# Kernel optimization log

Measured on AMD Instinct MI355X. Metric: run time of the kernel, lower is better.

The kernel has to match this reference:

```python
import math
import jax, jax.numpy as jnp
import numpy as np

B, S, DIM, H = 16, 1024, 1024, 16
HD = DIM // H            # head_dim = 64
ROPE_DIM = HD // 2       # 32; per-axis rotary dim
FT = 32                  # ft_seq_len, FT*FT == S
PT = 16                  # pt_seq_len
THETA = 10000.0
EPS = 1e-6


def _rope_cos_sin():
    # freqs_for='lang'
    freqs = 1.0 / THETA ** (jnp.arange(0, ROPE_DIM, 2, dtype=jnp.float32) / ROPE_DIM)  # [ROPE_DIM//2]
    t = jnp.arange(FT, dtype=jnp.float32) / FT * PT                                    # [FT]
    fs = jnp.einsum('n,f->nf', t, freqs)                                               # [FT, ROPE_DIM//2]
    fs = jnp.repeat(fs, 2, axis=-1)                                                    # [FT, ROPE_DIM]
    fh = jnp.broadcast_to(fs[:, None, :], (FT, FT, ROPE_DIM))
    fw = jnp.broadcast_to(fs[None, :, :], (FT, FT, ROPE_DIM))
    f = jnp.concatenate([fh, fw], axis=-1).reshape(-1, 2 * ROPE_DIM)                   # [S, HD]
    return jnp.cos(f), jnp.sin(f)


def _rotate_half(x):
    x1, x2 = jnp.split(x, 2, axis=-1)
    return jnp.concatenate((-x2, x1), axis=-1)


def _rms_norm(x, w):
    xf = x.astype(jnp.float32)
    var = jnp.mean(jnp.square(xf), axis=-1, keepdims=True)
    return (w * (xf * jax.lax.rsqrt(var + EPS))).astype(x.dtype)


def setup_inputs() -> dict:
    key = jax.random.key(0)
    ks = jax.random.split(key, 4)
    sd = 1.0 / math.sqrt(DIM)
    return {
        'x': jax.random.normal(ks[0], (B, S, DIM), dtype=jnp.float32),
        'w_qkv': jax.random.normal(ks[1], (DIM, 3 * DIM), dtype=jnp.float32) * sd,
        'b_qkv': jnp.zeros((3 * DIM,), dtype=jnp.float32),
        'q_norm_w': jnp.ones((HD,), dtype=jnp.float32),
        'k_norm_w': jnp.ones((HD,), dtype=jnp.float32),
        'w_out': jax.random.normal(ks[2], (DIM, DIM), dtype=jnp.float32) * sd,
        'b_out': jnp.zeros((DIM,), dtype=jnp.float32),
    }


def reference(x, w_qkv, b_qkv, q_norm_w, k_norm_w, w_out, b_out):
    cos, sin = _rope_cos_sin()                    # [S, HD] each
    cos = cos[None, None].astype(x.dtype)
    sin = sin[None, None].astype(x.dtype)

    qkv = x @ w_qkv + b_qkv                       # [B,S,3*DIM]
    qkv = qkv.reshape(B, S, 3, H, HD).transpose(2, 0, 3, 1, 4)  # [3,B,H,S,HD]
    q, k, v = qkv[0], qkv[1], qkv[2]

    q = _rms_norm(q, q_norm_w)
    k = _rms_norm(k, k_norm_w)

    q = q * cos + _rotate_half(q) * sin
    k = k * cos + _rotate_half(k) * sin

    scale = 1.0 / math.sqrt(HD)
    logits = jnp.einsum('bhqd,bhkd->bhqk', q.astype(jnp.float32), k.astype(jnp.float32)) * scale
    attn = jax.nn.softmax(logits, axis=-1).astype(x.dtype)
    out = jnp.einsum('bhqk,bhkd->bhqd', attn, v)  # [B,H,S,HD]

    out = out.transpose(0, 2, 1, 3).reshape(B, S, DIM)
    return out @ w_out + b_out
```

## Files before the change

kernel.cpp:

```cpp
#include <hip/hip_runtime.h>
#include <cstdint>
#include <cstddef>

#define B_    16
#define S_    1024
#define DIM_  1024
#define H_    16
#define HD_   64
#define TDIM  3072

typedef unsigned short ushort_t;
typedef unsigned int   uint_t;
typedef __attribute__((ext_vector_type(8)))  short s8v;
typedef __attribute__((ext_vector_type(4)))  float f32x4;
typedef __attribute__((ext_vector_type(16))) float f32x16;

__device__ __forceinline__ float b2f(ushort_t u) {
    union { uint_t i; float f; } t; t.i = (uint_t)u << 16; return t.f;
}
__device__ __forceinline__ ushort_t f2b(float f) {
    union { float f; uint_t i; } t; t.f = f;
    uint_t r = t.i + 0x7FFFu + ((t.i >> 16) & 1u);
    return (ushort_t)(r >> 16);
}
__device__ __forceinline__ uint_t cvt_pk_bf16(float a, float b) {
    uint_t r;
    asm("v_cvt_pk_bf16_f32 %0, %1, %2" : "=v"(r) : "v"(a), "v"(b));
    return r;
}

__device__ __forceinline__ f32x4 mfma_bf16(s8v a, s8v b, f32x4 c) {
    asm volatile("v_mfma_f32_16x16x32_bf16 %0, %1, %2, %0" : "+v"(c) : "v"(a), "v"(b));
    return c;
}
__device__ __forceinline__ f32x16 mfma32_bf16(s8v a, s8v b, f32x16 c) {
    asm volatile("v_mfma_f32_32x32x16_bf16 %0, %1, %2, %0" : "+v"(c) : "v"(a), "v"(b));
    return c;
}

__device__ __forceinline__ void gload16(const void* g, void* l) {
    __builtin_amdgcn_global_load_lds(
        (const __attribute__((address_space(1))) uint_t*)g,
        (__attribute__((address_space(3))) uint_t*)l, 16, 0, 0);
}

__device__ __forceinline__ void bar() {
    asm volatile("" ::: "memory");
    __builtin_amdgcn_s_barrier();
    asm volatile("" ::: "memory");
}
__device__ __forceinline__ void wait_vm0() {
    asm volatile("s_waitcnt vmcnt(0)" ::: "memory");
}
__device__ __forceinline__ void wait_vm4() {
    asm volatile("s_waitcnt vmcnt(4)" ::: "memory");
}

__global__ __launch_bounds__(256) void f32_to_bf16_vec(const float* __restrict__ src,
                                                       short* __restrict__ dst, int n8) {
    int i = blockIdx.x * 256 + threadIdx.x;
    if (i < n8) {
        float4 a = *(const float4*)(src + (size_t)i * 8);
        float4 b = *(const float4*)(src + (size_t)i * 8 + 4);
        s8v t;
        t[0] = (short)f2b(a.x); t[1] = (short)f2b(a.y);
        t[2] = (short)f2b(a.z); t[3] = (short)f2b(a.w);
        t[4] = (short)f2b(b.x); t[5] = (short)f2b(b.y);
        t[6] = (short)f2b(b.z); t[7] = (short)f2b(b.w);
        *(s8v*)(dst + (size_t)i * 8) = t;
    }
}

__global__ __launch_bounds__(256) void rope_tables(float* __restrict__ cos_t,
                                                   float* __restrict__ sin_t) {
    int idx = blockIdx.x * 256 + threadIdx.x;
    int s = idx >> 6;
    int d = idx & 63;
    int pos = (d < 32) ? (s >> 5) : (s & 31);
    int i   = (d & 31) >> 1;
    float freq  = expf(-(float)i * 0.5756462732485115f);
    float angle = (float)pos * 0.5f * freq;
    cos_t[idx] = cosf(angle);
    sin_t[idx] = sinf(angle);
}

__global__ __launch_bounds__(256) void transpose_to_bf16(const float* __restrict__ Wsrc,
                                                         short* __restrict__ WT,
                                                         int K, int N) {
    __shared__ float t[32][33];
    int tx = threadIdx.x & 31, ty = threadIdx.x >> 5;
    int n0 = blockIdx.x * 32, k0 = blockIdx.y * 32;
#pragma unroll
    for (int i = 0; i < 4; ++i)
        t[ty + 8 * i][tx] = Wsrc[(size_t)(k0 + ty + 8 * i) * N + n0 + tx];
    __syncthreads();
#pragma unroll
    for (int i = 0; i < 4; ++i)
        WT[(size_t)(n0 + ty + 8 * i) * K + k0 + tx] = (short)f2b(t[tx][ty + 8 * i]);
}

template<typename CT, bool NORM>
__global__ __launch_bounds__(512) void gemm8ph(
        const short* __restrict__ A, const short* __restrict__ BT,
        const float* __restrict__ bias, CT* __restrict__ C,
        int M, int N, int K, int NX,
        const float* __restrict__ qw, const float* __restrict__ kw,
        const float* __restrict__ cos_t, const float* __restrict__ sin_t) {
    __shared__ short As[2][256 * 64];
    __shared__ short Bs[3][256 * 64];

    const int tid  = threadIdx.x;
    const int w    = tid >> 6;
    const int lane = tid & 63;
    const int l15  = lane & 15, lg = lane >> 4;
    const int wm = w >> 2, wn = w & 3;

    const int nwg  = gridDim.x;
    const int cpx  = nwg >> 3;
    const int wgid = (blockIdx.x & 7) * cpx + (blockIdx.x >> 3);
    const int bx = wgid % NX, by = wgid / NX;
    const int m0 = by * 256, n0 = bx * 256;

    const int NT = K >> 6;

    const int sgrow = w * 8 + (lane >> 3);
    const int ksrc  = (((lane & 7) ^ (lane >> 3)) * 8);

    auto stageA = [&](int t, int buf) {
        const size_t k0 = (size_t)t * 64;
#pragma unroll
        for (int j = 0; j < 4; ++j)
            gload16(A + (size_t)(m0 + j * 64 + sgrow) * K + k0 + ksrc,
                    &As[buf][(j * 64 + w * 8) * 64]);
    };
    auto stageB = [&](int t, int buf) {
        const size_t k0 = (size_t)t * 64;
#pragma unroll
        for (int j = 0; j < 4; ++j)
            gload16(BT + (size_t)(n0 + j * 64 + sgrow) * K + k0 + ksrc,
                    &Bs[buf][(j * 64 + w * 8) * 64]);
    };

    const int swz = l15 & 7;

    auto rdA = [&](int buf, int mh, s8v (&dst)[4][2]) {
#pragma unroll
        for (int i = 0; i < 4; ++i) {
            int row = wm * 128 + mh * 64 + i * 16 + l15;
#pragma unroll
            for (int kk = 0; kk < 2; ++kk)
                dst[i][kk] = *(const s8v*)&As[buf][row * 64 + (((kk * 4 + lg) ^ swz) * 8)];
        }
    };
    auto rdB = [&](int buf, int nh, s8v (&dst)[4][2]) {
#pragma unroll
        for (int ni = 0; ni < 2; ++ni) {
            int row = wn * 64 + (nh * 2 + ni) * 16 + l15;
#pragma unroll
            for (int kk = 0; kk < 2; ++kk)
                dst[nh * 2 + ni][kk] = *(const s8v*)&Bs[buf][row * 64 + (((kk * 4 + lg) ^ swz) * 8)];
        }
    };

    stageA(0, 0);
    stageB(0, 0);
    stageB(1, 1);
    wait_vm4();
    bar();

    s8v a0[4][2], a1[4][2], bb[4][2];
    rdA(0, 0, a0);
    rdB(0, 0, bb);
    rdB(0, 1, bb);
    rdA(0, 1, a1);

    f32x4 acc[8][4] = {};

    int bufB = 0;
    for (int t = 0; t < NT; ++t) {
        const int bufA  = t & 1;
        const int nbufB = (bufB == 2) ? 0 : bufB + 1;
        const int sbufB = (nbufB == 2) ? 0 : nbufB + 1;

        if (t + 1 < NT) stageA(t + 1, bufA ^ 1);
        if (t + 2 < NT) stageB(t + 2, sbufB);

        __builtin_amdgcn_s_setprio(1);
#pragma unroll
        for (int i = 0; i < 4; ++i)
#pragma unroll
            for (int ni = 0; ni < 2; ++ni)
#pragma unroll
                for (int kk = 0; kk < 2; ++kk)
                    acc[i][ni] = mfma_bf16(a0[i][kk], bb[ni][kk], acc[i][ni]);
        __builtin_amdgcn_s_setprio(0);

        __builtin_amdgcn_s_setprio(1);
#pragma unroll
        for (int i = 0; i < 4; ++i)
#pragma unroll
            for (int ni = 2; ni < 4; ++ni)
#pragma unroll
                for (int kk = 0; kk < 2; ++kk)
                    acc[i][ni] = mfma_bf16(a0[i][kk], bb[ni][kk], acc[i][ni]);
        __builtin_amdgcn_s_setprio(0);

        __builtin_amdgcn_s_setprio(1);
#pragma unroll
        for (int i = 0; i < 4; ++i)
#pragma unroll
            for (int ni = 0; ni < 2; ++ni)
#pragma unroll
                for (int kk = 0; kk < 2; ++kk)
                    acc[4 + i][ni] = mfma_bf16(a1[i][kk], bb[ni][kk], acc[4 + i][ni]);
        __builtin_amdgcn_s_setprio(0);

        if (t < NT - 2) wait_vm4(); else wait_vm0();
        bar();

        if (t + 1 < NT) {
            rdA(bufA ^ 1, 0, a0);
            rdB(nbufB, 0, bb);
        }

        __builtin_amdgcn_s_setprio(1);
#pragma unroll
        for (int i = 0; i < 4; ++i)
#pragma unroll
            for (int ni = 2; ni < 4; ++ni)
#pragma unroll
                for (int kk = 0; kk < 2; ++kk)
                    acc[4 + i][ni] = mfma_bf16(a1[i][kk], bb[ni][kk], acc[4 + i][ni]);
        __builtin_amdgcn_s_setprio(0);

        if (t + 1 < NT) {
            rdB(nbufB, 1, bb);
            rdA(bufA ^ 1, 1, a1);
        }
        bufB = nbufB;
    }

    const int colbase = n0 + wn * 64;
    if constexpr (NORM) {
        if (colbase < 2048) {
            const float* nw = (colbase < 1024) ? qw : kw;
            float wv[4], bv[4];
#pragma unroll
            for (int ni = 0; ni < 4; ++ni) {
                wv[ni] = nw[16 * ni + l15];
                bv[ni] = bias[colbase + 16 * ni + l15];
            }
#pragma unroll
            for (int mi = 0; mi < 8; ++mi) {
#pragma unroll
                for (int r = 0; r < 4; ++r) {
                    int row = m0 + wm * 128 + mi * 16 + lg * 4 + r;
                    int s = row & (S_ - 1);
                    float v[4];
#pragma unroll
                    for (int ni = 0; ni < 4; ++ni) v[ni] = acc[mi][ni][r] + bv[ni];
                    float ss = v[0]*v[0] + v[1]*v[1] + v[2]*v[2] + v[3]*v[3];
                    ss += __shfl_xor(ss, 1);
                    ss += __shfl_xor(ss, 2);
                    ss += __shfl_xor(ss, 4);
                    ss += __shfl_xor(ss, 8);
                    float rms = rsqrtf(ss * (1.0f / 64.0f) + 1e-6f);
                    float xn[4];
#pragma unroll
                    for (int ni = 0; ni < 4; ++ni) xn[ni] = v[ni] * rms * wv[ni];
#pragma unroll
                    for (int ni = 0; ni < 4; ++ni) {
                        int d = 16 * ni + l15;
                        float c  = cos_t[s * 64 + d];
                        float sn = sin_t[s * 64 + d];
                        float rot = (ni < 2) ? -xn[ni + 2] : xn[ni - 2];
                        C[(size_t)row * N + colbase + d] = (short)f2b(xn[ni] * c + rot * sn);
                    }
                }
            }
            return;
        }
    }
#pragma unroll
    for (int ni = 0; ni < 4; ++ni) {
        float bvv = bias[colbase + 16 * ni + l15];
#pragma unroll
        for (int mi = 0; mi < 8; ++mi) {
#pragma unroll
            for (int r = 0; r < 4; ++r) {
                size_t row = (size_t)(m0 + wm * 128 + mi * 16 + lg * 4 + r);
                int    col = colbase + 16 * ni + l15;
                float v = acc[mi][ni][r] + bvv;
                if constexpr (sizeof(CT) == 4) C[row * N + col] = v;
                else                           C[row * N + col] = (short)f2b(v);
            }
        }
    }
}

__global__ __launch_bounds__(256) void attn_mfma(const short* __restrict__ qkv,
                                                 short* __restrict__ attn) {
    __shared__ ushort_t pool[8192];

    const float SC = 0.18033688011112042f;
    const float M_ = 12.0f;

    const int tid  = threadIdx.x;
    const int w    = tid >> 6;
    const int lane = tid & 63;
    const int l31  = lane & 31, l5 = lane >> 5;

    const int bid = blockIdx.x;
    const int xcd = bid & 7;
    const int jj_ = bid >> 3;
    const int bh  = xcd * 32 + (jj_ >> 3);
    const int b   = bh >> 4, h = bh & 15;
    const int q0  = (jj_ & 7) * 128;

    const short* qbase = qkv + (size_t)b * S_ * TDIM + h * HD_;
    const short* kb_ = qbase + DIM_;
    const short* vb_ = qbase + 2 * DIM_;

    ushort_t* Ks = pool;
    ushort_t* Vt = pool + 4096;

    s8v qf[4];
#pragma unroll
    for (int kc = 0; kc < 4; ++kc)
        qf[kc] = *(const s8v*)(qbase + (size_t)(q0 + w * 32 + l31) * TDIM + kc * 16 + l5 * 8);

    f32x16 of0 = {}, of1 = {};
    float l_s = 0.f;

    const int kr   = tid >> 3;
    const int kch  = (((tid & 7) ^ (kr & 7)) << 3);
    const int va   = tid & 7;
    const int vkp  = tid >> 3;
    const int vp8  = va * 8;
    const int k2    = 2 * vkp;
    const int kperm = (k2 & 0x33) | ((k2 & 4) << 1) | ((k2 & 8) >> 1);
    const int rsw   = l31 & 7;
    const int vrx   = (l31 & 7) ^ (l31 >> 3);

    s8v kA, kB, vA, vB;
    auto prefetch = [&](int kt) {
        const short* kbt = kb_ + (size_t)kt * 64 * TDIM;
        const short* vbt = vb_ + (size_t)kt * 64 * TDIM;
        kA = *(const s8v*)(kbt + (size_t)kr * TDIM + (tid & 7) * 8);
        kB = *(const s8v*)(kbt + (size_t)(kr + 32) * TDIM + (tid & 7) * 8);
        vA = *(const s8v*)(vbt + (size_t)k2 * TDIM + vp8);
        vB = *(const s8v*)(vbt + (size_t)(k2 + 1) * TDIM + vp8);
    };
    prefetch(0);

    for (int kt = 0; kt < 16; ++kt) {
        *(s8v*)&Ks[kr * 64 + kch]        = kA;
        *(s8v*)&Ks[(kr + 32) * 64 + kch] = kB;
#pragma unroll
        for (int j = 0; j < 8; ++j) {
            uint_t pk = (ushort_t)vA[j] | ((uint_t)(ushort_t)vB[j] << 16);
            int pcol = ((((kperm >> 3) ^ j ^ va) << 3) | (kperm & 7));
            *(uint_t*)&Vt[(vp8 + j) * 64 + pcol] = pk;
        }
        __syncthreads();

        if (kt < 15) prefetch(kt + 1);

        f32x16 st0 = {}, st1 = {};
        __builtin_amdgcn_s_setprio(1);
#pragma unroll
        for (int kc = 0; kc < 4; ++kc) {
            int pc = (((2 * kc + l5) ^ rsw) << 3);
            s8v kf0 = *(const s8v*)&Ks[l31 * 64 + pc];
            s8v kf1 = *(const s8v*)&Ks[(32 + l31) * 64 + pc];
            st0 = mfma32_bf16(kf0, qf[kc], st0);
            st1 = mfma32_bf16(kf1, qf[kc], st1);
        }
        __builtin_amdgcn_s_setprio(0);

        float la = 0.f, lb = 0.f, lc = 0.f, ld = 0.f;
#pragma unroll
        for (int r = 0; r < 16; r += 2) {
            float p00 = exp2f(__builtin_fmaf(st0[r],     SC, -M_));
            float p01 = exp2f(__builtin_fmaf(st0[r + 1], SC, -M_));
            float p10 = exp2f(__builtin_fmaf(st1[r],     SC, -M_));
            float p11 = exp2f(__builtin_fmaf(st1[r + 1], SC, -M_));
            st0[r] = p00; st0[r + 1] = p01;
            st1[r] = p10; st1[r + 1] = p11;
            la += p00; lb += p01; lc += p10; ld += p11;
        }
        float ls = (la + lb) + (lc + ld);
        ls += __shfl_xor(ls, 32);
        l_s += ls;

        uint_t P20[8], P21[8];
#pragma unroll
        for (int i = 0; i < 8; ++i) {
            P20[i] = cvt_pk_bf16(st0[2 * i], st0[2 * i + 1]);
            P21[i] = cvt_pk_bf16(st1[2 * i], st1[2 * i + 1]);
        }

        __builtin_amdgcn_s_setprio(1);
#pragma unroll
        for (int kb = 0; kb < 2; ++kb) {
            const uint_t* P2 = kb ? P21 : P20;
#pragma unroll
            for (int c = 0; c < 2; ++c) {
                union { uint_t u[4]; s8v v; } pf;
                pf.u[0] = P2[4 * c + 0];
                pf.u[1] = P2[4 * c + 1];
                pf.u[2] = P2[4 * c + 2];
                pf.u[3] = P2[4 * c + 3];

                int pc0 = (((4 * kb + 2 * c + l5) ^ vrx) << 3);
                int pc1 = pc0 ^ 32;
                s8v vf0 = *(const s8v*)&Vt[l31 * 64 + pc0];
                s8v vf1 = *(const s8v*)&Vt[(32 + l31) * 64 + pc1];
                of0 = mfma32_bf16(vf0, pf.v, of0);
                of1 = mfma32_bf16(vf1, pf.v, of1);
            }
        }
        __builtin_amdgcn_s_setprio(0);
        __syncthreads();
    }

    float inv = 1.0f / l_s;
    ushort_t* OL = pool + w * 2048;
#pragma unroll
    for (int r = 0; r < 16; r += 2) {
        int d = (r & 3) + 8 * (r >> 2) + 4 * l5;
        uint_t p0 = cvt_pk_bf16(of0[r] * inv, of0[r + 1] * inv);
        uint_t p1 = cvt_pk_bf16(of1[r] * inv, of1[r + 1] * inv);
        int c0 = d, c1 = 32 + d;
        int pc0 = (((c0 >> 3) ^ (l31 & 7)) << 3) | (c0 & 7);
        int pc1 = (((c1 >> 3) ^ (l31 & 7)) << 3) | (c1 & 7);
        *(uint_t*)&OL[l31 * 64 + pc0] = p0;
        *(uint_t*)&OL[l31 * 64 + pc1] = p1;
    }
#pragma unroll
    for (int i = 0; i < 4; ++i) {
        int idx = lane + i * 64;
        int row = idx >> 3, ch = idx & 7;
        int pch = ((ch ^ (row & 7)) << 3);
        *(s8v*)&attn[((size_t)b * S_ + q0 + w * 32 + row) * DIM_ + h * HD_ + ch * 8] =
            *(const s8v*)&OL[row * 64 + pch];
    }
}

extern "C" void kernel_launch(void* const* d_in, const int* in_sizes, int n_in,
                              void* d_out, int out_size, void* d_ws, size_t ws_size,
                              hipStream_t stream) {
    const float* x        = (const float*)d_in[0];
    const float* w_qkv    = (const float*)d_in[1];
    const float* b_qkv    = (const float*)d_in[2];
    const float* q_norm_w = (const float*)d_in[3];
    const float* k_norm_w = (const float*)d_in[4];
    const float* w_out    = (const float*)d_in[5];
    const float* b_out    = (const float*)d_in[6];
    float* out = (float*)d_out;

    const size_t OFF_QKV = 0;
    const size_t OFF_ATT = 100663296;
    const size_t OFF_XB  = OFF_ATT + 33554432;
    const size_t OFF_WQ  = OFF_XB + 33554432;
    const size_t OFF_WO  = OFF_WQ + 6291456;
    const size_t OFF_CT  = OFF_WO + 2097152;
    const size_t OFF_ST  = OFF_CT + 262144;
    const size_t NEED    = OFF_ST + 262144;

    if (ws_size < NEED) {
        hipMemsetAsync(d_out, 0, (size_t)out_size * sizeof(float), stream);
        return;
    }

    char* ws = (char*)d_ws;
    short* qkv   = (short*)(ws + OFF_QKV);
    short* attnb = (short*)(ws + OFF_ATT);
    short* xb    = (short*)(ws + OFF_XB);
    short* wqkvT = (short*)(ws + OFF_WQ);
    short* woutT = (short*)(ws + OFF_WO);
    float* cos_t = (float*)(ws + OFF_CT);
    float* sin_t = (float*)(ws + OFF_ST);

    rope_tables<<<dim3(256), dim3(256), 0, stream>>>(cos_t, sin_t);
    f32_to_bf16_vec<<<dim3(8192), dim3(256), 0, stream>>>(x, xb, 2097152);
    transpose_to_bf16<<<dim3(96, 32), dim3(256), 0, stream>>>(w_qkv, wqkvT, 1024, 3072);
    transpose_to_bf16<<<dim3(32, 32), dim3(256), 0, stream>>>(w_out, woutT, 1024, 1024);

    gemm8ph<short, true><<<dim3(768), dim3(512), 0, stream>>>(
        xb, wqkvT, b_qkv, qkv, 16384, 3072, 1024, 12,
        q_norm_w, k_norm_w, cos_t, sin_t);

    attn_mfma<<<dim3(2048), dim3(256), 0, stream>>>(qkv, attnb);

    gemm8ph<float, false><<<dim3(256), dim3(512), 0, stream>>>(
        attnb, woutT, b_out, out, 16384, 1024, 1024, 4,
        nullptr, nullptr, nullptr, nullptr);
}
```

Baseline: 283.2 us.

## Halve GEMM K-tile to 32 and triple-buffer both A and B in LDS

Shrinks the GEMM K-step from 64 to 32 and gives both A and B operands a three-deep LDS ring buffer, prefetching two tiles ahead. The barrier and wait move to the top of each iteration, and register fragment reloads are interleaved between MFMA groups. This is meant to cut LDS footprint, which may raise occupancy, and to deepen load/compute overlap. The cost is twice as many iterations and barriers per K sweep, with fewer MFMAs between each sync.

After: 297.9 us. +5.2%, slower.

```diff
diff --git a/kernel.cpp b/kernel.cpp
--- a/kernel.cpp
+++ b/kernel.cpp
@@ -106,8 +106,8 @@
         int M, int N, int K, int NX,
         const float* __restrict__ qw, const float* __restrict__ kw,
         const float* __restrict__ cos_t, const float* __restrict__ sin_t) {
-    __shared__ short As[2][256 * 64];
-    __shared__ short Bs[3][256 * 64];
+    __shared__ short As[3][256 * 32];
+    __shared__ short Bs[3][256 * 32];
 
     const int tid  = threadIdx.x;
     const int w    = tid >> 6;
@@ -121,78 +121,71 @@
     const int bx = wgid % NX, by = wgid / NX;
     const int m0 = by * 256, n0 = bx * 256;
 
-    const int NT = K >> 6;
-
-    const int sgrow = w * 8 + (lane >> 3);
-    const int ksrc  = (((lane & 7) ^ (lane >> 3)) * 8);
+    const int NT = K >> 5;
+
+    const int sgrow = w * 16 + (lane >> 2);
+    const int ksrc  = (((lane & 3) ^ ((lane >> 2) & 3)) * 8);
 
     auto stageA = [&](int t, int buf) {
-        const size_t k0 = (size_t)t * 64;
-#pragma unroll
-        for (int j = 0; j < 4; ++j)
-            gload16(A + (size_t)(m0 + j * 64 + sgrow) * K + k0 + ksrc,
-                    &As[buf][(j * 64 + w * 8) * 64]);
+        const size_t k0 = (size_t)t * 32;
+#pragma unroll
+        for (int j = 0; j < 2; ++j)
+            gload16(A + (size_t)(m0 + j * 128 + sgrow) * K + k0 + ksrc,
+                    &As[buf][(j * 128 + w * 16) * 32]);
     };
     auto stageB = [&](int t, int buf) {
-        const size_t k0 = (size_t)t * 64;
-#pragma unroll
-        for (int j = 0; j < 4; ++j)
-            gload16(BT + (size_t)(n0 + j * 64 + sgrow) * K + k0 + ksrc,
-                    &Bs[buf][(j * 64 + w * 8) * 64]);
+        const size_t k0 = (size_t)t * 32;
+#pragma unroll
+        for (int j = 0; j < 2; ++j)
+            gload16(BT + (size_t)(n0 + j * 128 + sgrow) * K + k0 + ksrc,
+                    &Bs[buf][(j * 128 + w * 16) * 32]);
     };
 
-    const int swz = l15 & 7;
-
-    auto rdA = [&](int buf, int mh, s8v (&dst)[4][2]) {
+    const int swz4 = l15 & 3;
+
+    auto rdA = [&](int buf, int mh, s8v (&dst)[4]) {
 #pragma unroll
         for (int i = 0; i < 4; ++i) {
             int row = wm * 128 + mh * 64 + i * 16 + l15;
-#pragma unroll
-            for (int kk = 0; kk < 2; ++kk)
-                dst[i][kk] = *(const s8v*)&As[buf][row * 64 + (((kk * 4 + lg) ^ swz) * 8)];
+            dst[i] = *(const s8v*)&As[buf][row * 32 + ((lg ^ swz4) * 8)];
         }
     };
-    auto rdB = [&](int buf, int nh, s8v (&dst)[4][2]) {
+    auto rdB2 = [&](int buf, int nh, s8v (&dst)[4]) {
 #pragma unroll
         for (int ni = 0; ni < 2; ++ni) {
             int row = wn * 64 + (nh * 2 + ni) * 16 + l15;
-#pragma unroll
-            for (int kk = 0; kk < 2; ++kk)
-                dst[nh * 2 + ni][kk] = *(const s8v*)&Bs[buf][row * 64 + (((kk * 4 + lg) ^ swz) * 8)];
+            dst[nh * 2 + ni] = *(const s8v*)&Bs[buf][row * 32 + ((lg ^ swz4) * 8)];
         }
     };
 
-    stageA(0, 0);
-    stageB(0, 0);
-    stageB(1, 1);
+    stageA(0, 0); stageB(0, 0);
+    stageA(1, 1); stageB(1, 1);
     wait_vm4();
     bar();
 
-    s8v a0[4][2], a1[4][2], bb[4][2];
+    s8v a0[4], a1[4], bb[4];
     rdA(0, 0, a0);
-    rdB(0, 0, bb);
-    rdB(0, 1, bb);
+    rdB2(0, 0, bb);
+    rdB2(0, 1, bb);
     rdA(0, 1, a1);
 
     f32x4 acc[8][4] = {};
 
-    int bufB = 0;
     for (int t = 0; t < NT; ++t) {
-        const int bufA  = t & 1;
-        const int nbufB = (bufB == 2) ? 0 : bufB + 1;
-        const int sbufB = (nbufB == 2) ? 0 : nbufB + 1;
-
-        if (t + 1 < NT) stageA(t + 1, bufA ^ 1);
-        if (t + 2 < NT) stageB(t + 2, sbufB);
+        const int b2 = (t + 2) % 3;
+        const int nb = (t + 1) % 3;
+        const bool more = (t + 1 < NT);
+
+        if (t + 2 < NT) { stageA(t + 2, b2); stageB(t + 2, b2); }
+        if (t + 2 < NT) wait_vm4(); else wait_vm0();
+        bar();
 
         __builtin_amdgcn_s_setprio(1);
 #pragma unroll
         for (int i = 0; i < 4; ++i)
 #pragma unroll
             for (int ni = 0; ni < 2; ++ni)
-#pragma unroll
-                for (int kk = 0; kk < 2; ++kk)
-                    acc[i][ni] = mfma_bf16(a0[i][kk], bb[ni][kk], acc[i][ni]);
+                acc[i][ni] = mfma_bf16(a0[i], bb[ni], acc[i][ni]);
         __builtin_amdgcn_s_setprio(0);
 
         __builtin_amdgcn_s_setprio(1);
@@ -200,44 +193,30 @@
         for (int i = 0; i < 4; ++i)
 #pragma unroll
             for (int ni = 2; ni < 4; ++ni)
-#pragma unroll
-                for (int kk = 0; kk < 2; ++kk)
-                    acc[i][ni] = mfma_bf16(a0[i][kk], bb[ni][kk], acc[i][ni]);
-        __builtin_amdgcn_s_setprio(0);
+                acc[i][ni] = mfma_bf16(a0[i], bb[ni], acc[i][ni]);
+        __builtin_amdgcn_s_setprio(0);
+
+        if (more) rdA(nb, 0, a0);
 
         __builtin_amdgcn_s_setprio(1);
 #pragma unroll
         for (int i = 0; i < 4; ++i)
 #pragma unroll
             for (int ni = 0; ni < 2; ++ni)
-#pragma unroll
-                for (int kk = 0; kk < 2; ++kk)
-                    acc[4 + i][ni] = mfma_bf16(a1[i][kk], bb[ni][kk], acc[4 + i][ni]);
-        __builtin_amdgcn_s_setprio(0);
-
-        if (t < NT - 2) wait_vm4(); else wait_vm0();
-        bar();
-
-        if (t + 1 < NT) {
-            rdA(bufA ^ 1, 0, a0);
-            rdB(nbufB, 0, bb);
-        }
+                acc[4 + i][ni] = mfma_bf16(a1[i], bb[ni], acc[4 + i][ni]);
+        __builtin_amdgcn_s_setprio(0);
+
+        if (more) rdB2(nb, 0, bb);
 
         __builtin_amdgcn_s_setprio(1);
 #pragma unroll
         for (int i = 0; i < 4; ++i)
 #pragma unroll
             for (int ni = 2; ni < 4; ++ni)
-#pragma unroll
-                for (int kk = 0; kk < 2; ++kk)
-                    acc[4 + i][ni] = mfma_bf16(a1[i][kk], bb[ni][kk], acc[4 + i][ni]);
-        __builtin_amdgcn_s_setprio(0);
-
-        if (t + 1 < NT) {
-            rdB(nbufB, 1, bb);
-            rdA(bufA ^ 1, 1, a1);
-        }
-        bufB = nbufB;
+                acc[4 + i][ni] = mfma_bf16(a1[i], bb[ni], acc[4 + i][ni]);
+        __builtin_amdgcn_s_setprio(0);
+
+        if (more) { rdB2(nb, 1, bb); rdA(nb, 1, a1); }
     }
 
     const int colbase = n0 + wn * 64;
```
